# Performance work log

Measured on AMD Instinct MI355X. Metric: run time of the kernel, lower is better.

## Reference

```python
import jax, jax.numpy as jnp
import numpy as np

E, H, VS, VT, B, S, T = 256, 512, 32000, 32000, 64, 40, 40

def setup_inputs() -> dict:
    key = jax.random.key(0)
    ks = jax.random.split(key, 32)
    def n(k, shape, scale=0.05):
        return (jax.random.normal(k, shape, jnp.float32) * scale)
    return {
        "source_padded": jax.random.randint(ks[0], (B, S), 0, VS),
        "target_padded": jax.random.randint(ks[1], (B, T), 0, VT),
        "source_lengths": jax.random.randint(ks[2], (B,), 2, S + 1),
        "src_emb": n(ks[3], (VS, E)), "tgt_emb": n(ks[4], (VT, E)),
        "Wih_f": n(ks[5], (4 * H, E)), "Whh_f": n(ks[6], (4 * H, H)), "b_f": jnp.zeros((4 * H,), jnp.float32),
        "Wih_b": n(ks[7], (4 * H, E)), "Whh_b": n(ks[8], (4 * H, H)), "b_b": jnp.zeros((4 * H,), jnp.float32),
        "Wih_d": n(ks[9], (4 * H, H + E)), "Whh_d": n(ks[10], (4 * H, H)), "b_d": jnp.zeros((4 * H,), jnp.float32),
        "Whp": n(ks[11], (H, 2 * H)), "bhp": jnp.zeros((H,), jnp.float32),
        "Wcp": n(ks[12], (H, 2 * H)), "bcp": jnp.zeros((H,), jnp.float32),
        "Watt": n(ks[13], (H, 2 * H)), "batt": jnp.zeros((H,), jnp.float32),
        "Wcomb": n(ks[14], (H, 3 * H)), "bcomb": jnp.zeros((H,), jnp.float32),
        "Wvoc": n(ks[15], (VT, H)), "bvoc": jnp.zeros((VT,), jnp.float32),
    }

def _lstm_cell(x, h, c, Wih, Whh, b):
    g = x @ Wih.T + h @ Whh.T + b
    i, f, gg, o = jnp.split(g, 4, axis=-1)  # PyTorch gate order i,f,g,o
    c = jax.nn.sigmoid(f) * c + jax.nn.sigmoid(i) * jnp.tanh(gg)
    h = jax.nn.sigmoid(o) * jnp.tanh(c)
    return h, c

def _masked_scan(X, lengths, Wih, Whh, b):
    # X: [B,S,E]; emulates packed LSTM: state frozen and output zeroed past length
    Bn, Sn, _ = X.shape
    Hn = Whh.shape[1]
    def step(carry, inp):
        h, c = carry
        xt, t = inp
        hn, cn = _lstm_cell(xt, h, c, Wih, Whh, b)
        valid = (t < lengths)[:, None]
        h = jnp.where(valid, hn, h)
        c = jnp.where(valid, cn, c)
        return (h, c), jnp.where(valid, h, 0.0)
    init = (jnp.zeros((Bn, Hn), X.dtype), jnp.zeros((Bn, Hn), X.dtype))
    (h, c), outs = jax.lax.scan(step, init, (X.transpose(1, 0, 2), jnp.arange(Sn)))
    return outs.transpose(1, 0, 2), h, c

def _rev_in_len(X, lengths):
    # reverse each sequence within its own length, zeros elsewhere
    Sn = X.shape[1]
    idx = lengths[:, None] - 1 - jnp.arange(Sn)[None, :]
    g = jnp.take_along_axis(X, jnp.clip(idx, 0)[..., None], axis=1)
    return jnp.where((idx >= 0)[..., None], g, 0.0)

def _forward(source_padded, target_padded, source_lengths,
             src_emb, tgt_emb, Wih_f, Whh_f, b_f, Wih_b, Whh_b, b_b,
             Wih_d, Whh_d, b_d, Whp, bhp, Wcp, bcp, Watt, batt,
             Wcomb, bcomb, Wvoc, bvoc):
    X = src_emb[source_padded]                              # [B,S,E]
    out_f, hf, cf = _masked_scan(X, source_lengths, Wih_f, Whh_f, b_f)
    Xr = _rev_in_len(X, source_lengths)
    out_r, hb, cb = _masked_scan(Xr, source_lengths, Wih_b, Whh_b, b_b)
    out_b = _rev_in_len(out_r, source_lengths)
    enc_hidden = jnp.concatenate([out_f, out_b], axis=-1)   # [B,S,2H]
    dec_h = jnp.concatenate([hf, hb], axis=-1) @ Whp.T + bhp
    dec_c = jnp.concatenate([cf, cb], axis=-1) @ Wcp.T + bcp

    # generate_sent_masks: 1 at positions 1..len-1 (faithful to source), then masked_fill(-inf) where 1
    pos = jnp.arange(S)[None, :]
    enc_masks = (pos >= 1) & (pos < source_lengths[:, None])  # [B,S] bool

    enc_proj = enc_hidden @ Watt.T + batt                    # [B,S,H]
    Y = tgt_emb[target_padded]                               # [B,T,E]
    Hn = Whh_d.shape[1]
    o0 = jnp.zeros((B, Hn), jnp.float32)

    def dec_step(carry, y_t):
        h, c, o_prev = carry
        ybar = jnp.concatenate([y_t, o_prev], axis=-1)
        h, c = _lstm_cell(ybar, h, c, Wih_d, Whh_d, b_d)
        e = jnp.einsum('bsh,bh->bs', enc_proj, h)
        e = jnp.where(enc_masks, -jnp.inf, e)
        alpha = jax.nn.softmax(e, axis=-1)
        a = jnp.einsum('bs,bsd->bd', alpha, enc_hidden)      # [B,2H]
        U = jnp.concatenate([h, a], axis=-1)                 # [B,3H]
        O = jnp.tanh(U @ Wcomb.T + bcomb)                    # dropout eval-mode identity
        return (h, c, O), O

    _, outs = jax.lax.scan(dec_step, (dec_h, dec_c, o0), Y.transpose(1, 0, 2))  # [T,B,H]
    logits = outs @ Wvoc.T + bvoc                            # [T,B,VT]
    logp = jax.nn.log_softmax(logits, axis=-1)
    # CrossEntropyLoss(P.permute(1,2,0), target): mean NLL over all B*T positions
    tgt = target_padded.T[..., None]                         # [T,B,1]
    nll = -jnp.take_along_axis(logp, tgt, axis=-1).squeeze(-1)
    return nll.mean()

def reference(source_padded, target_padded, source_lengths,
              src_emb, tgt_emb, Wih_f, Whh_f, b_f, Wih_b, Whh_b, b_b,
              Wih_d, Whh_d, b_d, Whp, bhp, Wcp, bcp, Watt, batt,
              Wcomb, bcomb, Wvoc, bvoc):
    return _forward(source_padded, target_padded, source_lengths,
                    src_emb, tgt_emb, Wih_f, Whh_f, b_f, Wih_b, Whh_b, b_b,
                    Wih_d, Whh_d, b_d, Whp, bhp, Wcp, bcp, Watt, batt,
                    Wcomb, bcomb, Wvoc, bvoc)
```

## Files before the change

kernel.cpp:

```cpp
#include <hip/hip_runtime.h>
#include <math.h>

#define En 256
#define Hn 512
#define Bn 64
#define Sn 40
#define Tn 40
#define VTn 32000
#define Rn (Tn*Bn)
#define NCH 500

typedef short v8s __attribute__((ext_vector_type(8)));
typedef float v4f __attribute__((ext_vector_type(4)));
typedef _Float16 h2v __attribute__((ext_vector_type(2)));

#if defined(__has_builtin)
#  if __has_builtin(__builtin_amdgcn_fdot2)
#    define HAVE_FDOT2 1
#  endif
#endif

__device__ __forceinline__ float dot4(float4 a, float4 b){
  return a.x*b.x + a.y*b.y + a.z*b.z + a.w*b.w;
}
__device__ __forceinline__ float sigm(float x){ return 1.f/(1.f+__expf(-x)); }
__device__ __forceinline__ unsigned short f2bf(float f){
  unsigned u = __float_as_uint(f);
  unsigned r = u + 0x7FFFu + ((u>>16)&1u);
  return (unsigned short)(r>>16);
}
__device__ __forceinline__ float bf2f(unsigned short u){
  return __uint_as_float(((unsigned)u)<<16);
}
__device__ __forceinline__ unsigned pkbf(float a, float b){
  return (unsigned)f2bf(a) | ((unsigned)f2bf(b)<<16);
}
__device__ __forceinline__ unsigned pkh(float a, float b){
  _Float16 ha = (_Float16)a, hb = (_Float16)b;
  unsigned short ua = __builtin_bit_cast(unsigned short, ha);
  unsigned short ub = __builtin_bit_cast(unsigned short, hb);
  return (unsigned)ua | ((unsigned)ub<<16);
}
__device__ __forceinline__ float fd2(unsigned w, unsigned h, float c){
#ifdef HAVE_FDOT2
  return __builtin_amdgcn_fdot2(__builtin_bit_cast(h2v,w), __builtin_bit_cast(h2v,h), c, false);
#else
  h2v a = __builtin_bit_cast(h2v,w), b = __builtin_bit_cast(h2v,h);
  return c + (float)a[0]*(float)b[0] + (float)a[1]*(float)b[1];
#endif
}

__global__ void prep(float* zero_base,
                     const int* __restrict__ src, const int* __restrict__ tgt,
                     const int* __restrict__ lens, int* __restrict__ grev,
                     int* __restrict__ gtgt,
                     const float* __restrict__ Whh_f, unsigned short* __restrict__ Whf16,
                     const float* __restrict__ Whh_b, unsigned short* __restrict__ Whb16,
                     const float* __restrict__ Whh_d, const float* __restrict__ Wih_d,
                     unsigned short* __restrict__ Wd16,
                     const float* __restrict__ Wcomb, unsigned short* __restrict__ Wc16){
  int blk = blockIdx.x, tid = threadIdx.x;
  if (blk < 224){
    ((float4*)zero_base)[blk*256 + tid] = make_float4(0.f,0.f,0.f,0.f);
    return;
  }
  blk -= 224;
  if (blk < 10){
    int r = blk*256 + tid;
    if (r < Bn*Sn){
      int b = r/Sn, s = r%Sn;
      int j = lens[b]-1-s;
      grev[r] = (j>=0) ? src[b*Sn+j] : -1;
      int t2 = r>>6, b2 = r&63;
      gtgt[r] = tgt[b2*Tn + t2];
    }
    return;
  }
  blk -= 10;
  if (blk < 512){
    size_t e = ((size_t)blk*256 + tid)*8;
    float4 a = *(const float4*)(Whh_f+e), b = *(const float4*)(Whh_f+e+4);
    uint4 u; u.x=pkbf(a.x,a.y); u.y=pkbf(a.z,a.w); u.z=pkbf(b.x,b.y); u.w=pkbf(b.z,b.w);
    *(uint4*)(Whf16+e) = u;
    return;
  }
  blk -= 512;
  if (blk < 512){
    size_t e = ((size_t)blk*256 + tid)*8;
    float4 a = *(const float4*)(Whh_b+e), b = *(const float4*)(Whh_b+e+4);
    uint4 u; u.x=pkbf(a.x,a.y); u.y=pkbf(a.z,a.w); u.z=pkbf(b.x,b.y); u.w=pkbf(b.z,b.w);
    *(uint4*)(Whb16+e) = u;
    return;
  }
  blk -= 512;
  if (blk < 1024){
    size_t e = ((size_t)blk*256 + tid)*8;
    int row = (int)(e>>10), k = (int)(e&1023);
    const float* sp = (k<512) ? (Whh_d + (size_t)row*512 + k)
                              : (Wih_d + (size_t)row*768 + 256 + (k-512));
    float4 a = *(const float4*)sp, b = *(const float4*)(sp+4);
    uint4 u; u.x=pkbf(a.x,a.y); u.y=pkbf(a.z,a.w); u.z=pkbf(b.x,b.y); u.w=pkbf(b.z,b.w);
    *(uint4*)(Wd16+e) = u;
    return;
  }
  blk -= 1024;
  {
    size_t e = ((size_t)blk*256 + tid)*8;
    float4 a = *(const float4*)(Wcomb+e), b = *(const float4*)(Wcomb+e+4);
    uint4 u; u.x=pkh(a.x,a.y); u.y=pkh(a.z,a.w); u.z=pkh(b.x,b.y); u.w=pkh(b.z,b.w);
    *(uint4*)(Wc16+e) = u;
  }
}

struct GArg {
  const float* A; const int* gth; int lda;
  const float* B; int ldb;
  const float* bias; float* C; int ldc; int K;
};
struct GArg3 { GArg a[3]; };

__global__ __launch_bounds__(256) void ggemm(GArg3 p3){
  GArg d = p3.a[blockIdx.z];
  __shared__ unsigned short Abf[128*64];
  __shared__ unsigned short Bbf[128*64];
  const int n0 = blockIdx.x*128, r0 = blockIdx.y*128;
  const int tid = threadIdx.x;
  const int w = tid>>6, lane = tid&63;
  const int wr = w>>1, wc = w&1;
  v4f acc[4][4];
#pragma unroll
  for (int i=0;i<4;++i)
#pragma unroll
    for (int j=0;j<4;++j) acc[i][j] = (v4f){0.f,0.f,0.f,0.f};
  const int srow = tid>>1, kc = (tid&1)*32;
  int ar = d.gth ? d.gth[r0+srow] : (r0+srow);
  const float* Arow = (ar>=0) ? (d.A + (size_t)ar*d.lda) : nullptr;
  const float* Brow = d.B + (size_t)(n0+srow)*d.ldb;
  for (int kb=0; kb<d.K; kb+=64){
    __syncthreads();
#pragma unroll
    for (int c=0;c<4;++c){
      int k = kc + c*8;
      int swz = k ^ ((srow&7)<<3);
      uint4 ua;
      if (Arow){
        float4 x0 = *(const float4*)(Arow+kb+k);
        float4 x1 = *(const float4*)(Arow+kb+k+4);
        ua.x=pkbf(x0.x,x0.y); ua.y=pkbf(x0.z,x0.w); ua.z=pkbf(x1.x,x1.y); ua.w=pkbf(x1.z,x1.w);
      } else ua = make_uint4(0,0,0,0);
      *(uint4*)&Abf[srow*64 + swz] = ua;
      float4 y0 = *(const float4*)(Brow+kb+k);
      float4 y1 = *(const float4*)(Brow+kb+k+4);
      uint4 ub; ub.x=pkbf(y0.x,y0.y); ub.y=pkbf(y0.z,y0.w); ub.z=pkbf(y1.x,y1.y); ub.w=pkbf(y1.z,y1.w);
      *(uint4*)&Bbf[srow*64 + swz] = ub;
    }
    __syncthreads();
#pragma unroll
    for (int kk=0; kk<64; kk+=32){
      int kfr = kk + (lane>>4)*8;
      v8s bfr[4];
#pragma unroll
      for (int ni=0;ni<4;++ni){
        int brow = wc*64 + ni*16 + (lane&15);
        bfr[ni] = *(const v8s*)&Bbf[brow*64 + (kfr ^ ((brow&7)<<3))];
      }
#pragma unroll
      for (int mi=0;mi<4;++mi){
        int arl = wr*64 + mi*16 + (lane&15);
        v8s af = *(const v8s*)&Abf[arl*64 + (kfr ^ ((arl&7)<<3))];
#pragma unroll
        for (int ni=0;ni<4;++ni)
          acc[mi][ni] = __builtin_amdgcn_mfma_f32_16x16x32_bf16(af, bfr[ni], acc[mi][ni], 0,0,0);
      }
    }
  }
#pragma unroll
  for (int ni=0;ni<4;++ni){
    int col = n0 + wc*64 + ni*16 + (lane&15);
    float bb = d.bias[col];
#pragma unroll
    for (int mi=0;mi<4;++mi)
#pragma unroll
      for (int r=0;r<4;++r){
        int row = r0 + wr*64 + mi*16 + (lane>>4)*4 + r;
        d.C[(size_t)row*d.ldc + col] = acc[mi][ni][r] + bb;
      }
  }
}

__global__ __launch_bounds__(256) void enc_step(
    const unsigned short* __restrict__ hf_in, unsigned short* __restrict__ hf_out,
    const unsigned short* __restrict__ hb_in, unsigned short* __restrict__ hb_out,
    float* __restrict__ cF, float* __restrict__ cB,
    const unsigned short* __restrict__ Wf16, const unsigned short* __restrict__ Wb16,
    const float* __restrict__ Gf, const float* __restrict__ Gb,
    float* __restrict__ encH, float* __restrict__ outR,
    const int* __restrict__ lens, int s){
  __shared__ unsigned short Wls[64*64];
  __shared__ unsigned short Hls[64*64];
  __shared__ float Cls[64][66];
  const int bx = blockIdx.x;
  const int dir = bx>>5;
  const int u0 = (bx&31)*16;
  const unsigned short* W16 = dir ? Wb16 : Wf16;
  const unsigned short* hin = dir ? hb_in : hf_in;
  unsigned short* hout      = dir ? hb_out : hf_out;
  float* c = dir ? cB : cF;
  const float* G = dir ? Gb : Gf;
  const int tid = threadIdx.x, w = tid>>6, lane = tid&63;
  v4f acc[4];
#pragma unroll
  for (int ni=0;ni<4;++ni) acc[ni] = (v4f){0.f,0.f,0.f,0.f};
  const int l = tid>>2;
  const int kc4 = (tid&3)*16;
  const int grow = (l>>4)*512 + u0 + (l&15);
  const unsigned short* Wrow = W16 + (size_t)grow*512;
  const unsigned short* Hrow = hin + (size_t)l*512;
  for (int kb=0; kb<512; kb+=64){
    __syncthreads();
#pragma unroll
    for (int c2=0;c2<2;++c2){
      int k = kc4 + c2*8;
      int swz = k ^ ((l&7)<<3);
      *(uint4*)&Wls[l*64+swz] = *(const uint4*)(Wrow + kb + k);
      *(uint4*)&Hls[l*64+swz] = *(const uint4*)(Hrow + kb + k);
    }
    __syncthreads();
#pragma unroll
    for (int kk=0; kk<64; kk+=32){
      int kfr = kk + (lane>>4)*8;
      int mrow = w*16 + (lane&15);
      v8s af = *(const v8s*)&Wls[mrow*64 + (kfr ^ ((mrow&7)<<3))];
#pragma unroll
      for (int ni=0;ni<4;++ni){
        int brow = ni*16 + (lane&15);
        v8s bf = *(const v8s*)&Hls[brow*64 + (kfr ^ ((brow&7)<<3))];
        acc[ni] = __builtin_amdgcn_mfma_f32_16x16x32_bf16(af, bf, acc[ni], 0,0,0);
      }
    }
  }
#pragma unroll
  for (int ni=0;ni<4;++ni)
#pragma unroll
    for (int r=0;r<4;++r)
      Cls[w*16 + (lane>>4)*4 + r][ni*16 + (lane&15)] = acc[ni][r];
  __syncthreads();
  const int u_l = tid&15, bq = tid>>4;
#pragma unroll
  for (int j=0;j<4;++j){
    int b = bq + j*16;
    size_t gidx = ((size_t)(b*Sn+s))*2048 + u0 + u_l;
    float gi = Cls[u_l][b]      + G[gidx];
    float gf = Cls[16+u_l][b]   + G[gidx+512];
    float gg = Cls[32+u_l][b]   + G[gidx+1024];
    float go = Cls[48+u_l][b]   + G[gidx+1536];
    int bu = b*512 + u0 + u_l;
    bool valid = s < lens[b];
    float cp = c[bu];
    float cn = sigm(gf)*cp + sigm(gi)*tanhf(gg);
    float hn = sigm(go)*tanhf(cn);
    c[bu] = valid ? cn : cp;
    hout[bu] = valid ? f2bf(hn) : hin[bu];
    if (dir==0) encH[((size_t)(b*Sn+s))*1024 + u0+u_l] = valid ? hn : 0.f;
    else        outR[((size_t)(b*Sn+s))*512  + u0+u_l] = valid ? hn : 0.f;
  }
}

__global__ void mid_fused(const unsigned short* __restrict__ h16f,
                          const unsigned short* __restrict__ h16b,
                          const float* __restrict__ cF, const float* __restrict__ cB,
                          const float* __restrict__ Whp, const float* __restrict__ bhp,
                          const float* __restrict__ Wcp, const float* __restrict__ bcp,
                          unsigned short* __restrict__ ho0, float* __restrict__ dC,
                          const float* __restrict__ outR, const int* __restrict__ lens,
                          float* __restrict__ encH,
                          const float* __restrict__ Wvoc, unsigned short* __restrict__ W16){
  int blk = blockIdx.x, tid = threadIdx.x;
  if (blk < 128){
    int isC = blk >= 64;
    int idx = (blk & 63)*256 + tid;
#pragma unroll
    for (int e=0;e<2;++e){
      int o = idx*2 + e;
      int b = o>>9, u = o&511;
      if (!isC){
        const float* wr = Whp + (size_t)u*1024;
        float acc = bhp[u];
        const uint4* hf4 = (const uint4*)(h16f + (size_t)b*512);
        for (int q=0;q<64;++q){
          uint4 v = hf4[q];
          unsigned uu[4] = {v.x,v.y,v.z,v.w};
#pragma unroll
          for (int i2=0;i2<4;++i2){
            acc += bf2f((unsigned short)(uu[i2]&0xFFFF))*wr[q*8+i2*2];
            acc += bf2f((unsigned short)(uu[i2]>>16))   *wr[q*8+i2*2+1];
          }
        }
        const uint4* hb4 = (const uint4*)(h16b + (size_t)b*512);
        const float* wr2 = wr + 512;
        for (int q=0;q<64;++q){
          uint4 v = hb4[q];
          unsigned uu[4] = {v.x,v.y,v.z,v.w};
#pragma unroll
          for (int i2=0;i2<4;++i2){
            acc += bf2f((unsigned short)(uu[i2]&0xFFFF))*wr2[q*8+i2*2];
            acc += bf2f((unsigned short)(uu[i2]>>16))   *wr2[q*8+i2*2+1];
          }
        }
        ho0[b*1024 + u] = f2bf(acc);
      } else {
        const float4* w4 = (const float4*)(Wcp + (size_t)u*1024);
        float acc = bcp[u];
        const float4* x1 = (const float4*)(cF + (size_t)b*512);
        const float4* x2 = (const float4*)(cB + (size_t)b*512);
        for (int q=0;q<128;++q) acc += dot4(x1[q], w4[q]);
        for (int q=0;q<128;++q) acc += dot4(x2[q], w4[128+q]);
        dC[b*512 + u] = acc;
      }
    }
    return;
  }
  blk -= 128;
  if (blk < 640){
    int e = (blk*256 + tid)*8;
    int u = e & 511;
    int bsi = e >> 9;
    int s = bsi % Sn, b = bsi / Sn;
    int len = lens[b];
    float4 v0 = make_float4(0,0,0,0), v1 = make_float4(0,0,0,0);
    if (s < len){
      int j = len-1-s;
      const float* sp = outR + ((size_t)(b*Sn+j))*512 + u;
      v0 = *(const float4*)sp; v1 = *(const float4*)(sp+4);
    }
    float* dp = encH + ((size_t)(b*Sn+s))*1024 + 512 + u;
    *(float4*)dp = v0; *(float4*)(dp+4) = v1;
    return;
  }
  blk -= 640;
  {
    size_t e = ((size_t)blk*256 + tid)*8;
    float4 a = *(const float4*)(Wvoc+e), b = *(const float4*)(Wvoc+e+4);
    uint4 u; u.x=pkbf(a.x,a.y); u.y=pkbf(a.z,a.w); u.z=pkbf(b.x,b.y); u.w=pkbf(b.z,b.w);
    *(uint4*)(W16+e) = u;
  }
}

__global__ __launch_bounds__(256) void dec_gates(
    const unsigned short* __restrict__ Wd16, const unsigned short* __restrict__ ho_cur,
    unsigned short* __restrict__ ho_next, const float* __restrict__ Gdy,
    float* __restrict__ dC, int t){
  __shared__ unsigned short Wls[64*64];
  __shared__ unsigned short Hls[64*64];
  __shared__ float Cls[64][66];
  const int u0 = blockIdx.x*16;
  const int tid = threadIdx.x, w = tid>>6, lane = tid&63;
  v4f acc[4];
#pragma unroll
  for (int ni=0;ni<4;++ni) acc[ni] = (v4f){0.f,0.f,0.f,0.f};
  const int l = tid>>2;
  const int kc4 = (tid&3)*16;
  const int grow = (l>>4)*512 + u0 + (l&15);
  const unsigned short* Wrow = Wd16 + (size_t)grow*1024;
  const unsigned short* Hrow = ho_cur + (size_t)l*1024;
  for (int kb=0; kb<1024; kb+=64){
    __syncthreads();
#pragma unroll
    for (int c2=0;c2<2;++c2){
      int k = kc4 + c2*8;
      int swz = k ^ ((l&7)<<3);
      *(uint4*)&Wls[l*64+swz] = *(const uint4*)(Wrow + kb + k);
      *(uint4*)&Hls[l*64+swz] = *(const uint4*)(Hrow + kb + k);
    }
    __syncthreads();
#pragma unroll
    for (int kk=0; kk<64; kk+=32){
      int kfr = kk + (lane>>4)*8;
      int mrow = w*16 + (lane&15);
      v8s af = *(const v8s*)&Wls[mrow*64 + (kfr ^ ((mrow&7)<<3))];
#pragma unroll
      for (int ni=0;ni<4;++ni){
        int brow = ni*16 + (lane&15);
        v8s bf = *(const v8s*)&Hls[brow*64 + (kfr ^ ((brow&7)<<3))];
        acc[ni] = __builtin_amdgcn_mfma_f32_16x16x32_bf16(af, bf, acc[ni], 0,0,0);
      }
    }
  }
#pragma unroll
  for (int ni=0;ni<4;++ni)
#pragma unroll
    for (int r=0;r<4;++r)
      Cls[w*16 + (lane>>4)*4 + r][ni*16 + (lane&15)] = acc[ni][r];
  __syncthreads();
  const int u_l = tid&15, bq = tid>>4;
#pragma unroll
  for (int j=0;j<4;++j){
    int b = bq + j*16;
    size_t gidx = ((size_t)(t*Bn+b))*2048 + u0 + u_l;
    float gi = Cls[u_l][b]      + Gdy[gidx];
    float gf = Cls[16+u_l][b]   + Gdy[gidx+512];
    float gg = Cls[32+u_l][b]   + Gdy[gidx+1024];
    float go = Cls[48+u_l][b]   + Gdy[gidx+1536];
    int bu = b*512 + u0 + u_l;
    float cp = dC[bu];
    float cn = sigm(gf)*cp + sigm(gi)*tanhf(gg);
    float hn = sigm(go)*tanhf(cn);
    dC[bu] = cn;
    ho_next[b*1024 + u0 + u_l] = f2bf(hn);
  }
}

__global__ __launch_bounds__(256) void dec_attcomb(
    unsigned short* __restrict__ ho_next, const float* __restrict__ eprj,
    const float* __restrict__ encH, const int* __restrict__ lens,
    const unsigned short* __restrict__ Wc16, const float* __restrict__ bcomb,
    unsigned short* __restrict__ A16, int t){
  const int b = blockIdx.x >> 2;
  const int q = blockIdx.x & 3;
  const int tid = threadIdx.x;
  __shared__ __align__(16) float hs[512];
  __shared__ __align__(16) float als[1024];
  __shared__ float es[Sn], sal[Sn];
  __shared__ float sinv;
  __shared__ __align__(16) unsigned int ha16[768];
  __shared__ float ps[128][2];
  for (int i=tid; i<512; i+=256) hs[i] = bf2f(ho_next[b*1024 + i]);
  __syncthreads();
  const int wv = tid>>6, lane = tid&63;
  const int len = lens[b];
  for (int si=0; si<10; ++si){
    int s2 = wv*10 + si;
    const float* pr = eprj + ((size_t)(b*Sn+s2))*512 + lane*8;
    float4 p0 = *(const float4*)pr, p1 = *(const float4*)(pr+4);
    const float* hh = hs + lane*8;
    float4 h0 = *(const float4*)hh, h1 = *(const float4*)(hh+4);
    float a = dot4(p0,h0) + dot4(p1,h1);
#pragma unroll
    for (int off=32; off; off>>=1) a += __shfl_down(a, off);
    if (lane==0) es[s2] = (s2>=1 && s2<len) ? -INFINITY : a;
  }
  __syncthreads();
  if (tid < 64){
    float e2 = (tid<Sn) ? es[tid] : -INFINITY;
    float m = e2;
#pragma unroll
    for (int off=32; off; off>>=1) m = fmaxf(m, __shfl_xor(m, off));
    float p = (tid<Sn) ? __expf(e2-m) : 0.f;
    float sum = p;
#pragma unroll
    for (int off=32; off; off>>=1) sum += __shfl_xor(sum, off);
    if (tid<Sn) sal[tid] = p;
    if (tid==0) sinv = 1.f/sum;
  }
  __syncthreads();
  float inv = sinv;
#pragma unroll
  for (int dq=0; dq<4; ++dq){
    int d = dq*256 + tid;
    float acc = 0.f;
    for (int s2=0; s2<Sn; ++s2) acc += sal[s2]*encH[((size_t)(b*Sn+s2))*1024 + d];
    als[d] = acc*inv;
  }
  __syncthreads();
  for (int p=tid; p<768; p+=256){
    int i0 = 2*p, i1 = 2*p+1;
    float x0 = (i0<512) ? hs[i0] : als[i0-512];
    float x1 = (i1<512) ? hs[i1] : als[i1-512];
    ha16[p] = pkh(x0, x1);
  }
  __syncthreads();
  const int rloc = tid & 127;
  const int kh = tid >> 7;
  const int row = q*128 + rloc;
  const uint4* wp = (const uint4*)(Wc16 + (size_t)row*1536 + kh*768);
  const uint4* hp = (const uint4*)&ha16[kh*384];
  float a0 = 0.f;
#pragma unroll 4
  for (int qq=0; qq<96; ++qq){
    uint4 wv4 = wp[qq];
    uint4 hv4 = hp[qq];
    a0 = fd2(wv4.x, hv4.x, a0);
    a0 = fd2(wv4.y, hv4.y, a0);
    a0 = fd2(wv4.z, hv4.z, a0);
    a0 = fd2(wv4.w, hv4.w, a0);
  }
  ps[rloc][kh] = a0;
  __syncthreads();
  if (tid < 128){
    int r2 = q*128 + tid;
    float O = tanhf(ps[tid][0] + ps[tid][1] + bcomb[r2]);
    unsigned short ob = f2bf(O);
    ho_next[b*1024 + 512 + r2] = ob;
    A16[((size_t)(t*Bn+b))*512 + r2] = ob;
  }
}

__global__ __launch_bounds__(256,1) void vocab_mfma(
    const unsigned short* __restrict__ A16, const unsigned short* __restrict__ W16,
    const float* __restrict__ bv, float* __restrict__ stats){
  __shared__ unsigned short Abf[256*64];
  __shared__ unsigned short Bbf[128*64];
  const int vb = blockIdx.x, rb = blockIdx.y;
  const int r0 = rb*256, v0 = vb*128;
  const int tid = threadIdx.x, w = tid>>6, lane = tid&63;
  const int wr = w>>1, wc = w&1;
  v4f acc[8][4];
#pragma unroll
  for (int i=0;i<8;++i)
#pragma unroll
    for (int j=0;j<4;++j) acc[i][j] = (v4f){0.f,0.f,0.f,0.f};
  const unsigned short* Arow = A16 + (size_t)(r0+tid)*512;
  const int srow2 = tid>>1, kc2 = (tid&1)*32;
  const unsigned short* Brow = W16 + (size_t)(v0+srow2)*512;
  for (int kb=0; kb<512; kb+=64){
    __syncthreads();
#pragma unroll
    for (int c=0;c<8;++c){
      int k = c*8;
      *(uint4*)&Abf[tid*64 + (k ^ ((tid&7)<<3))] = *(const uint4*)(Arow + kb + k);
    }
#pragma unroll
    for (int c=0;c<4;++c){
      int k = kc2 + c*8;
      *(uint4*)&Bbf[srow2*64 + (k ^ ((srow2&7)<<3))] = *(const uint4*)(Brow + kb + k);
    }
    __syncthreads();
#pragma unroll
    for (int kk=0; kk<64; kk+=32){
      int kfr = kk + (lane>>4)*8;
      v8s bfr[4];
#pragma unroll
      for (int ni=0;ni<4;++ni){
        int brow = wc*64 + ni*16 + (lane&15);
        bfr[ni] = *(const v8s*)&Bbf[brow*64 + (kfr ^ ((brow&7)<<3))];
      }
#pragma unroll
      for (int mi=0;mi<8;++mi){
        int arow = wr*128 + mi*16 + (lane&15);
        v8s af = *(const v8s*)&Abf[arow*64 + (kfr ^ ((arow&7)<<3))];
#pragma unroll
        for (int ni=0;ni<4;++ni)
          acc[mi][ni] = __builtin_amdgcn_mfma_f32_16x16x32_bf16(af, bfr[ni], acc[mi][ni], 0,0,0);
      }
    }
  }
  float bj[4];
#pragma unroll
  for (int ni=0;ni<4;++ni) bj[ni] = bv[v0 + wc*64 + ni*16 + (lane&15)];
#pragma unroll
  for (int mi=0;mi<8;++mi){
#pragma unroll
    for (int r=0;r<4;++r){
      float x0 = acc[mi][0][r]+bj[0], x1 = acc[mi][1][r]+bj[1];
      float x2 = acc[mi][2][r]+bj[2], x3 = acc[mi][3][r]+bj[3];
      float mx = fmaxf(fmaxf(x0,x1), fmaxf(x2,x3));
#pragma unroll
      for (int off=1; off<16; off<<=1) mx = fmaxf(mx, __shfl_xor(mx, off));
      float se = __expf(x0-mx)+__expf(x1-mx)+__expf(x2-mx)+__expf(x3-mx);
#pragma unroll
      for (int off=1; off<16; off<<=1) se += __shfl_xor(se, off);
      if ((lane&15)==0){
        int row = r0 + wr*128 + mi*16 + (lane>>4)*4 + r;
        int chunk = vb*2 + wc;
        size_t o = ((size_t)row*NCH + chunk)*2;
        stats[o] = mx; stats[o+1] = se;
      }
    }
  }
}

__global__ void tail(const float* __restrict__ stats, const unsigned short* __restrict__ A16,
                     const float* __restrict__ Wvoc, const float* __restrict__ bvoc,
                     const int* __restrict__ gtgt, float* __restrict__ out){
  int r = blockIdx.x*4 + (threadIdx.x>>6);
  int lane = threadIdx.x & 63;
  const float* st = stats + (size_t)r*NCH*2;
  float M = -INFINITY;
  for (int c=lane; c<NCH; c+=64) M = fmaxf(M, st[2*c]);
#pragma unroll
  for (int off=32; off; off>>=1) M = fmaxf(M, __shfl_xor(M, off));
  float S = 0.f;
  for (int c=lane; c<NCH; c+=64) S += __expf(st[2*c]-M)*st[2*c+1];
#pragma unroll
  for (int off=32; off; off>>=1) S += __shfl_xor(S, off);
  int v = gtgt[r];
  int k = lane*8;
  uint4 a4 = *(const uint4*)(A16 + (size_t)r*512 + k);
  const float* wvp = Wvoc + (size_t)v*512 + k;
  float4 w0 = *(const float4*)wvp, w1 = *(const float4*)(wvp+4);
  unsigned uu[4] = {a4.x, a4.y, a4.z, a4.w};
  float dot = 0.f;
  dot += bf2f((unsigned short)(uu[0]&0xFFFF))*w0.x + bf2f((unsigned short)(uu[0]>>16))*w0.y;
  dot += bf2f((unsigned short)(uu[1]&0xFFFF))*w0.z + bf2f((unsigned short)(uu[1]>>16))*w0.w;
  dot += bf2f((unsigned short)(uu[2]&0xFFFF))*w1.x + bf2f((unsigned short)(uu[2]>>16))*w1.y;
  dot += bf2f((unsigned short)(uu[3]&0xFFFF))*w1.z + bf2f((unsigned short)(uu[3]>>16))*w1.w;
#pragma unroll
  for (int off=32; off; off>>=1) dot += __shfl_down(dot, off);
  if (lane==0){
    float lse = M + logf(S);
    float nll = lse - (dot + bvoc[v]);
    atomicAdd(out, nll * (1.0f/(float)Rn));
  }
}

extern "C" void kernel_launch(void* const* d_in, const int* in_sizes, int n_in,
                              void* d_out, int out_size, void* d_ws, size_t ws_size,
                              hipStream_t stream){
  (void)in_sizes; (void)n_in; (void)out_size; (void)ws_size;
  const int*   srcP  = (const int*)  d_in[0];
  const int*   tgtP  = (const int*)  d_in[1];
  const int*   lens  = (const int*)  d_in[2];
  const float* semb  = (const float*)d_in[3];
  const float* temb  = (const float*)d_in[4];
  const float* Wih_f = (const float*)d_in[5];
  const float* Whh_f = (const float*)d_in[6];
  const float* b_f   = (const float*)d_in[7];
  const float* Wih_b = (const float*)d_in[8];
  const float* Whh_b = (const float*)d_in[9];
  const float* b_b   = (const float*)d_in[10];
  const float* Wih_d = (const float*)d_in[11];
  const float* Whh_d = (const float*)d_in[12];
  const float* b_d   = (const float*)d_in[13];
  const float* Whp   = (const float*)d_in[14];
  const float* bhp   = (const float*)d_in[15];
  const float* Wcp   = (const float*)d_in[16];
  const float* bcp   = (const float*)d_in[17];
  const float* Watt  = (const float*)d_in[18];
  const float* batt  = (const float*)d_in[19];
  const float* Wcomb = (const float*)d_in[20];
  const float* bcomb = (const float*)d_in[21];
  const float* Wvoc  = (const float*)d_in[22];
  const float* bvoc  = (const float*)d_in[23];

  float* w = (float*)d_ws;
  size_t off = 0;
  auto alloc = [&](size_t n){ float* p = w + off; off += n; return p; };
  float* encH = alloc(2621440);
  float* outR = alloc(1310720);
  float* eprj = alloc(1310720);
  float* Gf   = alloc(5242880);
  float* Gb   = alloc(5242880);
  float* Gdy  = alloc(5242880);
  unsigned short* A16   = (unsigned short*)alloc(655360);
  unsigned short* Whf16 = (unsigned short*)alloc(524288);
  unsigned short* Whb16 = (unsigned short*)alloc(524288);
  unsigned short* Wd16  = (unsigned short*)alloc(1048576);
  unsigned short* Wc16  = (unsigned short*)alloc(393216);
  float* zero_base = w + off;
  float* cF = alloc(32768);
  float* cB = alloc(32768);
  float* dC = alloc(32768);
  unsigned short* h16f[2] = {(unsigned short*)alloc(16384), (unsigned short*)alloc(16384)};
  unsigned short* h16b[2] = {(unsigned short*)alloc(16384), (unsigned short*)alloc(16384)};
  unsigned short* ho[2]   = {(unsigned short*)alloc(32768), (unsigned short*)alloc(32768)};
  int* grev = (int*)alloc(2560);
  int* gtgt = (int*)alloc(2560);
  unsigned short* W16 = (unsigned short*)Gf;
  float* stats = encH;

  hipMemsetAsync(d_out, 0, sizeof(float), stream);
  prep<<<2666, 256, 0, stream>>>(zero_base, srcP, tgtP, lens, grev, gtgt,
                                 Whh_f, Whf16, Whh_b, Whb16, Whh_d, Wih_d, Wd16,
                                 Wcomb, Wc16);
  {
    GArg3 g;
    g.a[0] = GArg{semb, srcP, En, Wih_f, En,  b_f, Gf,  2048, En};
    g.a[1] = GArg{semb, grev, En, Wih_b, En,  b_b, Gb,  2048, En};
    g.a[2] = GArg{temb, gtgt, En, Wih_d, 768, b_d, Gdy, 2048, En};
    ggemm<<<dim3(16,20,3), 256, 0, stream>>>(g);
  }
  for (int s=0; s<Sn; ++s)
    enc_step<<<64, 256, 0, stream>>>(h16f[s&1], h16f[(s+1)&1], h16b[s&1], h16b[(s+1)&1],
                                     cF, cB, Whf16, Whb16, Gf, Gb, encH, outR, lens, s);
  mid_fused<<<8768, 256, 0, stream>>>(h16f[0], h16b[0], cF, cB, Whp, bhp, Wcp, bcp,
                                      ho[0], dC, outR, lens, encH, Wvoc, W16);
  {
    GArg3 g;
    g.a[0] = GArg{encH, nullptr, 1024, Watt, 1024, batt, eprj, 512, 1024};
    g.a[1] = g.a[0]; g.a[2] = g.a[0];
    ggemm<<<dim3(4,20,1), 256, 0, stream>>>(g);
  }
  for (int t=0; t<Tn; ++t){
    dec_gates<<<32, 256, 0, stream>>>(Wd16, ho[t&1], ho[(t+1)&1], Gdy, dC, t);
    dec_attcomb<<<256, 256, 0, stream>>>(ho[(t+1)&1], eprj, encH, lens, Wc16, bcomb, A16, t);
  }
  vocab_mfma<<<dim3(VTn/128, Rn/256), 256, 0, stream>>>(A16, W16, bvoc, stats);
  tail<<<Rn/4, 256, 0, stream>>>(stats, A16, Wvoc, bvoc, gtgt, (float*)d_out);
}
```

Baseline: 2.440 ms.

## Overlap Wvoc bf16 conversion with encoder steps and retile vocab GEMM

```diff
diff --git a/kernel.cpp b/kernel.cpp
--- a/kernel.cpp
+++ b/kernel.cpp
@@ -60,11 +60,11 @@
                      unsigned short* __restrict__ Wd16,
                      const float* __restrict__ Wcomb, unsigned short* __restrict__ Wc16){
   int blk = blockIdx.x, tid = threadIdx.x;
-  if (blk < 224){
+  if (blk < 209){
     ((float4*)zero_base)[blk*256 + tid] = make_float4(0.f,0.f,0.f,0.f);
     return;
   }
-  blk -= 224;
+  blk -= 209;
   if (blk < 10){
     int r = blk*256 + tid;
     if (r < Bn*Sn){
@@ -195,26 +195,39 @@
     const unsigned short* __restrict__ Wf16, const unsigned short* __restrict__ Wb16,
     const float* __restrict__ Gf, const float* __restrict__ Gb,
     float* __restrict__ encH, float* __restrict__ outR,
-    const int* __restrict__ lens, int s){
+    const int* __restrict__ lens,
+    const float* __restrict__ Wvoc, unsigned short* __restrict__ W16, int s){
+  const int bxall = blockIdx.x;
+  const int tid = threadIdx.x;
+  if (bxall >= 64){
+    int chunk = s*200 + (bxall - 64);
+    if (chunk < 8000){
+      size_t e = ((size_t)chunk*256 + tid)*8;
+      float4 a = *(const float4*)(Wvoc+e), b = *(const float4*)(Wvoc+e+4);
+      uint4 u; u.x=pkbf(a.x,a.y); u.y=pkbf(a.z,a.w); u.z=pkbf(b.x,b.y); u.w=pkbf(b.z,b.w);
+      *(uint4*)(W16+e) = u;
+    }
+    return;
+  }
   __shared__ unsigned short Wls[64*64];
   __shared__ unsigned short Hls[64*64];
   __shared__ float Cls[64][66];
-  const int bx = blockIdx.x;
+  const int bx = bxall;
   const int dir = bx>>5;
   const int u0 = (bx&31)*16;
-  const unsigned short* W16 = dir ? Wb16 : Wf16;
+  const unsigned short* Wm16 = dir ? Wb16 : Wf16;
   const unsigned short* hin = dir ? hb_in : hf_in;
   unsigned short* hout      = dir ? hb_out : hf_out;
   float* c = dir ? cB : cF;
   const float* G = dir ? Gb : Gf;
-  const int tid = threadIdx.x, w = tid>>6, lane = tid&63;
+  const int w = tid>>6, lane = tid&63;
   v4f acc[4];
 #pragma unroll
   for (int ni=0;ni<4;++ni) acc[ni] = (v4f){0.f,0.f,0.f,0.f};
   const int l = tid>>2;
   const int kc4 = (tid&3)*16;
   const int grow = (l>>4)*512 + u0 + (l&15);
-  const unsigned short* Wrow = W16 + (size_t)grow*512;
+  const unsigned short* Wrow = Wm16 + (size_t)grow*512;
   const unsigned short* Hrow = hin + (size_t)l*512;
   for (int kb=0; kb<512; kb+=64){
     __syncthreads();
@@ -273,8 +286,7 @@
                           const float* __restrict__ Wcp, const float* __restrict__ bcp,
                           unsigned short* __restrict__ ho0, float* __restrict__ dC,
                           const float* __restrict__ outR, const int* __restrict__ lens,
-                          float* __restrict__ encH,
-                          const float* __restrict__ Wvoc, unsigned short* __restrict__ W16){
+                          float* __restrict__ encH){
   int blk = blockIdx.x, tid = threadIdx.x;
   if (blk < 128){
     int isC = blk >= 64;
@@ -321,7 +333,7 @@
     return;
   }
   blk -= 128;
-  if (blk < 640){
+  {
     int e = (blk*256 + tid)*8;
     int u = e & 511;
     int bsi = e >> 9;
@@ -335,14 +347,6 @@
     }
     float* dp = encH + ((size_t)(b*Sn+s))*1024 + 512 + u;
     *(float4*)dp = v0; *(float4*)(dp+4) = v1;
-    return;
-  }
-  blk -= 640;
-  {
-    size_t e = ((size_t)blk*256 + tid)*8;
-    float4 a = *(const float4*)(Wvoc+e), b = *(const float4*)(Wvoc+e+4);
-    uint4 u; u.x=pkbf(a.x,a.y); u.y=pkbf(a.z,a.w); u.z=pkbf(b.x,b.y); u.w=pkbf(b.z,b.w);
-    *(uint4*)(W16+e) = u;
   }
 }
 
@@ -495,60 +499,64 @@
   }
 }
 
-__global__ __launch_bounds__(256,1) void vocab_mfma(
+__global__ __launch_bounds__(256) void vocab_mfma(
     const unsigned short* __restrict__ A16, const unsigned short* __restrict__ W16,
     const float* __restrict__ bv, float* __restrict__ stats){
-  __shared__ unsigned short Abf[256*64];
+  __shared__ unsigned short Abf[128*64];
   __shared__ unsigned short Bbf[128*64];
   const int vb = blockIdx.x, rb = blockIdx.y;
-  const int r0 = rb*256, v0 = vb*128;
-  const int tid = threadIdx.x, w = tid>>6, lane = tid&63;
+  const int r0 = rb*128, v0 = vb*128;
+  const int tid = threadIdx.x;
+  const int w = tid>>6, lane = tid&63;
   const int wr = w>>1, wc = w&1;
-  v4f acc[8][4];
-#pragma unroll
-  for (int i=0;i<8;++i)
+  v4f acc[4][4];
+#pragma unroll
+  for (int i=0;i<4;++i)
 #pragma unroll
     for (int j=0;j<4;++j) acc[i][j] = (v4f){0.f,0.f,0.f,0.f};
-  const unsigned short* Arow = A16 + (size_t)(r0+tid)*512;
-  const int srow2 = tid>>1, kc2 = (tid&1)*32;
-  const unsigned short* Brow = W16 + (size_t)(v0+srow2)*512;
-  for (int kb=0; kb<512; kb+=64){
+  const int srow = tid>>1;
+  const int sk0  = (tid&1)*8;
+  const int arow = wr*64 + (lane&15);
+  const int brow = wc*64 + (lane&15);
+  const int kfrag = (lane>>4)*8;
+  for (int ks=0; ks<8; ++ks){
+    const int kb = ks*64;
     __syncthreads();
 #pragma unroll
-    for (int c=0;c<8;++c){
-      int k = c*8;
-      *(uint4*)&Abf[tid*64 + (k ^ ((tid&7)<<3))] = *(const uint4*)(Arow + kb + k);
-    }
-#pragma unroll
     for (int c=0;c<4;++c){
-      int k = kc2 + c*8;
-      *(uint4*)&Bbf[srow2*64 + (k ^ ((srow2&7)<<3))] = *(const uint4*)(Brow + kb + k);
+      int k = sk0 + c*16;
+      int swz = k ^ ((srow&7)<<3);
+      *(uint4*)&Abf[srow*64 + swz] = *(const uint4*)(A16 + (size_t)(r0+srow)*512 + kb + k);
+      *(uint4*)&Bbf[srow*64 + swz] = *(const uint4*)(W16 + (size_t)(v0+srow)*512 + kb + k);
     }
     __syncthreads();
 #pragma unroll
     for (int kk=0; kk<64; kk+=32){
-      int kfr = kk + (lane>>4)*8;
-      v8s bfr[4];
+      v8s af[4], bf[4];
+#pragma unroll
+      for (int mi=0;mi<4;++mi){
+        int row = arow + mi*16;
+        int k = kk + kfrag;
+        af[mi] = *(const v8s*)&Abf[row*64 + (k ^ ((row&7)<<3))];
+      }
 #pragma unroll
       for (int ni=0;ni<4;++ni){
-        int brow = wc*64 + ni*16 + (lane&15);
-        bfr[ni] = *(const v8s*)&Bbf[brow*64 + (kfr ^ ((brow&7)<<3))];
-      }
-#pragma unroll
-      for (int mi=0;mi<8;++mi){
-        int arow = wr*128 + mi*16 + (lane&15);
-        v8s af = *(const v8s*)&Abf[arow*64 + (kfr ^ ((arow&7)<<3))];
+        int row = brow + ni*16;
+        int k = kk + kfrag;
+        bf[ni] = *(const v8s*)&Bbf[row*64 + (k ^ ((row&7)<<3))];
+      }
+#pragma unroll
+      for (int mi=0;mi<4;++mi)
 #pragma unroll
         for (int ni=0;ni<4;++ni)
-          acc[mi][ni] = __builtin_amdgcn_mfma_f32_16x16x32_bf16(af, bfr[ni], acc[mi][ni], 0,0,0);
-      }
+          acc[mi][ni] = __builtin_amdgcn_mfma_f32_16x16x32_bf16(af[mi], bf[ni], acc[mi][ni], 0,0,0);
     }
   }
   float bj[4];
 #pragma unroll
   for (int ni=0;ni<4;++ni) bj[ni] = bv[v0 + wc*64 + ni*16 + (lane&15)];
 #pragma unroll
-  for (int mi=0;mi<8;++mi){
+  for (int mi=0;mi<4;++mi){
 #pragma unroll
     for (int r=0;r<4;++r){
       float x0 = acc[mi][0][r]+bj[0], x1 = acc[mi][1][r]+bj[1];
@@ -560,10 +568,11 @@
 #pragma unroll
       for (int off=1; off<16; off<<=1) se += __shfl_xor(se, off);
       if ((lane&15)==0){
-        int row = r0 + wr*128 + mi*16 + (lane>>4)*4 + r;
+        int row = r0 + wr*64 + mi*16 + (lane>>4)*4 + r;
         int chunk = vb*2 + wc;
         size_t o = ((size_t)row*NCH + chunk)*2;
-        stats[o] = mx; stats[o+1] = se;
+        stats[o]   = mx;
+        stats[o+1] = se;
       }
     }
   }
@@ -641,6 +650,7 @@
   float* Gf   = alloc(5242880);
   float* Gb   = alloc(5242880);
   float* Gdy  = alloc(5242880);
+  unsigned short* W16   = (unsigned short*)alloc((size_t)VTn*Hn/2);
   unsigned short* A16   = (unsigned short*)alloc(655360);
   unsigned short* Whf16 = (unsigned short*)alloc(524288);
   unsigned short* Whb16 = (unsigned short*)alloc(524288);
@@ -650,16 +660,18 @@
   float* cF = alloc(32768);
   float* cB = alloc(32768);
   float* dC = alloc(32768);
-  unsigned short* h16f[2] = {(unsigned short*)alloc(16384), (unsigned short*)alloc(16384)};
-  unsigned short* h16b[2] = {(unsigned short*)alloc(16384), (unsigned short*)alloc(16384)};
-  unsigned short* ho[2]   = {(unsigned short*)alloc(32768), (unsigned short*)alloc(32768)};
+  unsigned short* h16f0 = (unsigned short*)alloc(16384);
+  unsigned short* h16f1 = (unsigned short*)alloc(16384);
+  unsigned short* h16b0 = (unsigned short*)alloc(16384);
+  unsigned short* h16b1 = (unsigned short*)alloc(16384);
+  unsigned short* ho0   = (unsigned short*)alloc(32768);
+  unsigned short* ho1   = (unsigned short*)alloc(32768);
   int* grev = (int*)alloc(2560);
   int* gtgt = (int*)alloc(2560);
-  unsigned short* W16 = (unsigned short*)Gf;
   float* stats = encH;
 
   hipMemsetAsync(d_out, 0, sizeof(float), stream);
-  prep<<<2666, 256, 0, stream>>>(zero_base, srcP, tgtP, lens, grev, gtgt,
+  prep<<<2651, 256, 0, stream>>>(zero_base, srcP, tgtP, lens, grev, gtgt,
                                  Whh_f, Whf16, Whh_b, Whb16, Whh_d, Wih_d, Wd16,
                                  Wcomb, Wc16);
   {
@@ -669,21 +681,28 @@
     g.a[2] = GArg{temb, gtgt, En, Wih_d, 768, b_d, Gdy, 2048, En};
     ggemm<<<dim3(16,20,3), 256, 0, stream>>>(g);
   }
-  for (int s=0; s<Sn; ++s)
-    enc_step<<<64, 256, 0, stream>>>(h16f[s&1], h16f[(s+1)&1], h16b[s&1], h16b[(s+1)&1],
-                                     cF, cB, Whf16, Whb16, Gf, Gb, encH, outR, lens, s);
-  mid_fused<<<8768, 256, 0, stream>>>(h16f[0], h16b[0], cF, cB, Whp, bhp, Wcp, bcp,
-                                      ho[0], dC, outR, lens, encH, Wvoc, W16);
+  for (int s=0; s<Sn; ++s){
+    const unsigned short* hfi = (s&1) ? h16f1 : h16f0;
+    unsigned short*       hfo = (s&1) ? h16f0 : h16f1;
+    const unsigned short* hbi = (s&1) ? h16b1 : h16b0;
+    unsigned short*       hbo = (s&1) ? h16b0 : h16b1;
+    enc_step<<<264, 256, 0, stream>>>(hfi, hfo, hbi, hbo, cF, cB,
+                                      Whf16, Whb16, Gf, Gb, encH, outR, lens,
+                                      Wvoc, W16, s);
+  }
+  mid_fused<<<768, 256, 0, stream>>>(h16f0, h16b0, cF, cB, Whp, bhp, Wcp, bcp,
+                                     ho0, dC, outR, lens, encH);
   {
     GArg3 g;
     g.a[0] = GArg{encH, nullptr, 1024, Watt, 1024, batt, eprj, 512, 1024};
     g.a[1] = g.a[0]; g.a[2] = g.a[0];
     ggemm<<<dim3(4,20,1), 256, 0, stream>>>(g);
   }
+  unsigned short* Hb[2] = {ho0, ho1};
   for (int t=0; t<Tn; ++t){
-    dec_gates<<<32, 256, 0, stream>>>(Wd16, ho[t&1], ho[(t+1)&1], Gdy, dC, t);
-    dec_attcomb<<<256, 256, 0, stream>>>(ho[(t+1)&1], eprj, encH, lens, Wc16, bcomb, A16, t);
-  }
-  vocab_mfma<<<dim3(VTn/128, Rn/256), 256, 0, stream>>>(A16, W16, bvoc, stats);
+    dec_gates<<<32, 256, 0, stream>>>(Wd16, Hb[t&1], Hb[(t+1)&1], Gdy, dC, t);
+    dec_attcomb<<<256, 256, 0, stream>>>(Hb[(t+1)&1], eprj, encH, lens, Wc16, bcomb, A16, t);
+  }
+  vocab_mfma<<<dim3(VTn/128, Rn/128), 256, 0, stream>>>(A16, W16, bvoc, stats);
   tail<<<Rn/4, 256, 0, stream>>>(stats, A16, Wvoc, bvoc, gtgt, (float*)d_out);
 }
```

Measured after the change: 2.284 ms (median of 2 runs). -6.4%, faster.
